# Optimization experiments

Measured on AMD Instinct MI355X. Metric: run time of the kernel, lower is better.

The kernel has to match this reference:

```python
import jax, jax.numpy as jnp
import numpy as np

B, H, W, C = 8, 256, 256, 64
M1, M2 = 16, 16
WIDTH = 64
W_SCALE = 0.02  # mimics he-normal-ish init magnitude for complex spectral weights


def setup_inputs() -> dict:
    key = jax.random.key(0)
    k1, k2, k3 = jax.random.split(key, 3)
    x = jax.random.normal(k1, (B, H, W, C), dtype=jnp.float32)
    w_real = jax.random.normal(k2, (M1, M2, C, WIDTH), dtype=jnp.float32)
    w_imag = jax.random.normal(k3, (M1, M2, C, WIDTH), dtype=jnp.float32)
    return {"x": x, "w_real": w_real, "w_imag": w_imag}


def reference(x, w_real, w_imag):
    # complex spectral weights: (M1, M2, C_in, C_out)
    weights = (w_real + 1j * w_imag) * W_SCALE
    spatial = x.shape[1:-1]  # (H, W)
    # full real FFT over spatial axes -> (B, H, W//2+1, C) complex
    x_ft = jnp.fft.rfftn(x, axes=(1, 2))
    # truncate to low-frequency modes
    x_m = x_ft[:, :M1, :M2, :]  # (B, M1, M2, C)
    # per-mode channel mixing (broadcast-ellipsis einsum in the original)
    out_m = jnp.einsum("bxyi,xyio->bxyo", x_m, weights)  # (B, M1, M2, WIDTH)
    # zero-pad back to full spectral grid
    pad = ((0, 0), (0, x_ft.shape[1] - M1), (0, x_ft.shape[2] - M2), (0, 0))
    out_ft = jnp.pad(out_m, pad, mode="constant")
    # inverse real FFT back to spatial domain
    out = jnp.fft.irfftn(out_ft, s=spatial, axes=(1, 2))  # (B, H, W, WIDTH)
    return out
```

## Files before the change

### kernel.cpp

```cpp
#include <hip/hip_runtime.h>


#define NB 8
#define NH 256
#define NW 256
#define NC 64
#define NM 16
#define NO 64

__global__ __launch_bounds__(256) void k_dft_w(const float* __restrict__ x,
                                               float* __restrict__ Gr, float* __restrict__ Gi) {
  __shared__ float2 cs[256];
  __shared__ float xs[4 * 1040];
  const int t = threadIdx.x;
  const int b = blockIdx.x >> 6;
  const int h0 = (blockIdx.x & 63) * 4;
  {
    float s, c;
    sincospif((float)t * (1.0f / 128.0f), &s, &c);
    cs[t] = make_float2(c, s);
  }
  const int i4 = t & 15;
  const int hs = (t >> 4) & 3;
  const int kyq = t >> 6;

  float4 ar[4], ai[4];
#pragma unroll
  for (int q = 0; q < 4; ++q) { ar[q] = make_float4(0, 0, 0, 0); ai[q] = make_float4(0, 0, 0, 0); }
  float stepr[4], stepi[4], twr[4], twi[4];

  const float* xb = x + (((size_t)b * NH + h0) * NW) * NC;

  for (int ch = 0; ch < 16; ++ch) {
    const int w0 = ch * 16;
    __syncthreads();
#pragma unroll
    for (int r = 0; r < 4; ++r) {
      const float4* src = (const float4*)(xb + ((size_t)r * NW + w0) * NC);
      ((float4*)xs)[r * 260 + t] = src[t];
    }
    __syncthreads();
    if (ch == 0) {
#pragma unroll
      for (int q = 0; q < 4; ++q) {
        const int ky = kyq * 4 + q;
        float2 st = cs[ky];
        stepr[q] = st.x; stepi[q] = -st.y;
      }
    }
#pragma unroll
    for (int q = 0; q < 4; ++q) {
      const int ky = kyq * 4 + q;
      float2 tv = cs[(ky * w0) & 255];
      twr[q] = tv.x; twi[q] = -tv.y;
    }
#pragma unroll 4
    for (int ww = 0; ww < 16; ++ww) {
      float4 xv = ((const float4*)xs)[hs * 260 + ww * 16 + i4];
#pragma unroll
      for (int q = 0; q < 4; ++q) {
        ar[q].x += twr[q] * xv.x; ar[q].y += twr[q] * xv.y;
        ar[q].z += twr[q] * xv.z; ar[q].w += twr[q] * xv.w;
        ai[q].x += twi[q] * xv.x; ai[q].y += twi[q] * xv.y;
        ai[q].z += twi[q] * xv.z; ai[q].w += twi[q] * xv.w;
        float nr = twr[q] * stepr[q] - twi[q] * stepi[q];
        float ni = twr[q] * stepi[q] + twi[q] * stepr[q];
        twr[q] = nr; twi[q] = ni;
      }
    }
  }
  const int h = h0 + hs;
#pragma unroll
  for (int q = 0; q < 4; ++q) {
    const int ky = kyq * 4 + q;
    const size_t o = (((size_t)(b * NM + ky)) * NH + h) * NC + i4 * 4;
    *(float4*)(Gr + o) = ar[q];
    *(float4*)(Gi + o) = ai[q];
  }
}

__global__ __launch_bounds__(256) void k_dft_h(const float* __restrict__ Gr, const float* __restrict__ Gi,
                                               float* __restrict__ Xr, float* __restrict__ Xi) {
  __shared__ float2 cs[256];
  __shared__ float gr[64 * 36];
  __shared__ float gi[64 * 36];
  const int t = threadIdx.x;
  const int b = blockIdx.x >> 5;
  const int ky = (blockIdx.x >> 1) & 15;
  const int ih = blockIdx.x & 1;
  {
    float s, c;
    sincospif((float)t * (1.0f / 128.0f), &s, &c);
    cs[t] = make_float2(c, s);
  }
  const int kx = t >> 4;
  const int i2 = (t & 15) * 2;
  float2 xr = make_float2(0, 0), xi = make_float2(0, 0);
  float str = 0.f, sti = 0.f, twr, twi;
  const float* grb = Gr + ((size_t)(b * NM + ky)) * NH * NC + ih * 32;
  const float* gib = Gi + ((size_t)(b * NM + ky)) * NH * NC + ih * 32;
  for (int ch = 0; ch < 4; ++ch) {
    const int h0 = ch * 64;
    __syncthreads();
    for (int r = 0; r < 2; ++r) {
      const int idx = r * 256 + t;
      const int hh = idx >> 3, f4 = idx & 7;
      ((float4*)&gr[hh * 36])[f4] = *(const float4*)(grb + (size_t)(h0 + hh) * NC + f4 * 4);
      ((float4*)&gi[hh * 36])[f4] = *(const float4*)(gib + (size_t)(h0 + hh) * NC + f4 * 4);
    }
    __syncthreads();
    if (ch == 0) { float2 st = cs[kx]; str = st.x; sti = -st.y; }
    float2 tv = cs[(kx * h0) & 255];
    twr = tv.x; twi = -tv.y;
#pragma unroll 8
    for (int hh = 0; hh < 64; ++hh) {
      float2 g_r = *(const float2*)&gr[hh * 36 + i2];
      float2 g_i = *(const float2*)&gi[hh * 36 + i2];
      xr.x += twr * g_r.x - twi * g_i.x;
      xr.y += twr * g_r.y - twi * g_i.y;
      xi.x += twr * g_i.x + twi * g_r.x;
      xi.y += twr * g_i.y + twi * g_r.y;
      float nr = twr * str - twi * sti;
      float ni = twr * sti + twi * str;
      twr = nr; twi = ni;
    }
  }
  const size_t o = ((size_t)((kx * NM + ky) * NB + b)) * NC + ih * 32 + i2;
  *(float2*)(Xr + o) = xr;
  *(float2*)(Xi + o) = xi;
}

__global__ __launch_bounds__(256) void k_mix(const float* __restrict__ Xr, const float* __restrict__ Xi,
                                             const float* __restrict__ w_real, const float* __restrict__ w_imag,
                                             float* __restrict__ omr, float* __restrict__ omi) {
  __shared__ float wr[64 * 64];
  __shared__ float wi[64 * 64];
  __shared__ float2 xc[8 * 64];
  const int t = threadIdx.x;
  const int kx = blockIdx.x >> 4;
  const int ky = blockIdx.x & 15;
  const size_t wbase = (size_t)(kx * NM + ky) * 4096;
  const float4* s1 = (const float4*)(w_real + wbase);
  const float4* s2 = (const float4*)(w_imag + wbase);
#pragma unroll
  for (int r = 0; r < 4; ++r) {
    ((float4*)wr)[r * 256 + t] = s1[r * 256 + t];
    ((float4*)wi)[r * 256 + t] = s2[r * 256 + t];
  }
  const size_t xbase = (size_t)(kx * NM + ky) * 512;
  for (int idx = t; idx < 512; idx += 256)
    xc[idx] = make_float2(Xr[xbase + idx], Xi[xbase + idx]);
  __syncthreads();
  const int b = t >> 5;
  const int o2 = (t & 31) * 2;
  float r0 = 0, i0 = 0, r1 = 0, i1 = 0;
#pragma unroll 8
  for (int i = 0; i < 64; ++i) {
    float2 xv = xc[b * 64 + i];
    float2 w_r = *(const float2*)&wr[i * 64 + o2];
    float2 w_i = *(const float2*)&wi[i * 64 + o2];
    r0 += xv.x * w_r.x - xv.y * w_i.x;
    i0 += xv.x * w_i.x + xv.y * w_r.x;
    r1 += xv.x * w_r.y - xv.y * w_i.y;
    i1 += xv.x * w_i.y + xv.y * w_r.y;
  }
  const float scale = (ky == 0 ? 1.0f : 2.0f) * (0.02f / 65536.0f);
  const size_t ob = (size_t)((b * NM + kx) * NM + ky) * NO + o2;
  *(float2*)(omr + ob) = make_float2(r0 * scale, r1 * scale);
  *(float2*)(omi + ob) = make_float2(i0 * scale, i1 * scale);
}

__global__ __launch_bounds__(256) void k_idft_w(const float* __restrict__ omr, const float* __restrict__ omi,
                                                float2* __restrict__ Zc) {
  __shared__ float2 cs[256];
  const int t = threadIdx.x;
  const int b = blockIdx.x >> 5;
  const int kx = (blockIdx.x >> 1) & 15;
  const int wh = blockIdx.x & 1;
  {
    float s, c;
    sincospif((float)t * (1.0f / 128.0f), &s, &c);
    cs[t] = make_float2(c, s);
  }
  __syncthreads();
  const int o = t & 63;
  const int wv = t >> 6;
  float mr[16], mi[16];
  const size_t base = (size_t)(b * NM + kx) * (NM * NO) + o;
#pragma unroll
  for (int ky = 0; ky < 16; ++ky) {
    mr[ky] = omr[base + ky * NO];
    mi[ky] = omi[base + ky * NO];
  }
  for (int j = 0; j < 32; ++j) {
    const int w = wh * 128 + wv * 32 + j;
    const float2 st = cs[w];
    float twr = 1.0f, twi = 0.0f;
    float zr = 0.0f, zi = 0.0f;
#pragma unroll
    for (int ky = 0; ky < 16; ++ky) {
      zr += twr * mr[ky] - twi * mi[ky];
      zi += twr * mi[ky] + twi * mr[ky];
      float nr = twr * st.x - twi * st.y;
      float ni = twr * st.y + twi * st.x;
      twr = nr; twi = ni;
    }
    Zc[((size_t)(b * NW + w) * NM + kx) * NO + o] = make_float2(zr, zi);
  }
}

__global__ __launch_bounds__(256) void k_idft_h(const float2* __restrict__ Zc, float* __restrict__ out) {
  __shared__ float2 cs[256];
  __shared__ float2 zc[16 * 64];
  const int t = threadIdx.x;
  const int b = blockIdx.x >> 8;
  const int w = blockIdx.x & 255;
  {
    float s, c;
    sincospif((float)t * (1.0f / 128.0f), &s, &c);
    cs[t] = make_float2(c, s);
  }
  {
    const float4* src = (const float4*)(Zc + (size_t)(b * NW + w) * (NM * NO));
    ((float4*)zc)[t] = src[t];
    ((float4*)zc)[t + 256] = src[t + 256];
  }
  __syncthreads();
  const int i4 = t & 15;
  const int h0 = (t >> 4) * 16;
  float4 acc[16];
#pragma unroll
  for (int j = 0; j < 16; ++j) acc[j] = make_float4(0, 0, 0, 0);
  for (int kx = 0; kx < 16; ++kx) {
    const float4 za = ((const float4*)zc)[kx * 32 + i4 * 2];
    const float4 zb = ((const float4*)zc)[kx * 32 + i4 * 2 + 1];
    const float2 t0 = cs[(kx * h0) & 255];
    const float2 st = cs[kx];
    float twr = t0.x, twi = t0.y;
#pragma unroll
    for (int j = 0; j < 16; ++j) {
      acc[j].x += twr * za.x - twi * za.y;
      acc[j].y += twr * za.z - twi * za.w;
      acc[j].z += twr * zb.x - twi * zb.y;
      acc[j].w += twr * zb.z - twi * zb.w;
      float nr = twr * st.x - twi * st.y;
      float ni = twr * st.y + twi * st.x;
      twr = nr; twi = ni;
    }
  }
  float* ob = out + (((size_t)b * NH + h0) * NW + w) * NO + i4 * 4;
#pragma unroll
  for (int j = 0; j < 16; ++j) {
    *(float4*)(ob + (size_t)j * (NW * NO)) = acc[j];
  }
}

extern "C" void kernel_launch(void* const* d_in, const int* in_sizes, int n_in,
                              void* d_out, int out_size, void* d_ws, size_t ws_size,
                              hipStream_t stream) {
  const float* x = (const float*)d_in[0];
  const float* w_real = (const float*)d_in[1];
  const float* w_imag = (const float*)d_in[2];
  float* out = (float*)d_out;
  char* ws = (char*)d_ws;

  float* Gr = (float*)(ws);
  float* Gi = (float*)(ws + 8388608);
  float* Xr = (float*)(ws + 16777216);
  float* Xi = (float*)(ws + 17301504);
  float* omr = (float*)(ws + 17825792);
  float* omi = (float*)(ws + 18350080);
  float2* Zc = (float2*)(ws + 18874368);

  k_dft_w<<<dim3(512), dim3(256), 0, stream>>>(x, Gr, Gi);
  k_dft_h<<<dim3(256), dim3(256), 0, stream>>>(Gr, Gi, Xr, Xi);
  k_mix<<<dim3(256), dim3(256), 0, stream>>>(Xr, Xi, w_real, w_imag, omr, omi);
  k_idft_w<<<dim3(256), dim3(256), 0, stream>>>(omr, omi, Zc);
  k_idft_h<<<dim3(2048), dim3(256), 0, stream>>>(Zc, out);
}
```

Baseline: 333.5 us.

## Raise grid parallelism across all DFT stages with split-H partial sums

Every stage is re-partitioned to launch more blocks. The W-DFT drops its LDS staging and reads x directly with fewer modes per thread. The H-DFT is split into 8 H-chunks that write partial sums, which the mix kernel reduces. The mix and inverse kernels are split in half or quarters along output channel, W and H, and complex intermediates are interleaved and reuse workspace. The aim is better occupancy on a GPU that was under-filled with 256-block launches, at the cost of extra partial-sum traffic and reduced per-thread reuse.

Result: faster. 311.5 us (-6.6%).

```diff
diff --git a/kernel.cpp b/kernel.cpp
--- a/kernel.cpp
+++ b/kernel.cpp
@@ -11,198 +11,177 @@
 __global__ __launch_bounds__(256) void k_dft_w(const float* __restrict__ x,
                                                float* __restrict__ Gr, float* __restrict__ Gi) {
   __shared__ float2 cs[256];
-  __shared__ float xs[4 * 1040];
-  const int t = threadIdx.x;
-  const int b = blockIdx.x >> 6;
-  const int h0 = (blockIdx.x & 63) * 4;
-  {
-    float s, c;
-    sincospif((float)t * (1.0f / 128.0f), &s, &c);
-    cs[t] = make_float2(c, s);
-  }
+  const int t = threadIdx.x;
+  {
+    float s, c;
+    sincospif((float)t * (1.0f / 128.0f), &s, &c);
+    cs[t] = make_float2(c, s);
+  }
+  __syncthreads();
+  const int b = blockIdx.x >> 7;
+  const int h2 = blockIdx.x & 127;
   const int i4 = t & 15;
-  const int hs = (t >> 4) & 3;
-  const int kyq = t >> 6;
-
-  float4 ar[4], ai[4];
-#pragma unroll
-  for (int q = 0; q < 4; ++q) { ar[q] = make_float4(0, 0, 0, 0); ai[q] = make_float4(0, 0, 0, 0); }
-  float stepr[4], stepi[4], twr[4], twi[4];
-
-  const float* xb = x + (((size_t)b * NH + h0) * NW) * NC;
-
-  for (int ch = 0; ch < 16; ++ch) {
-    const int w0 = ch * 16;
-    __syncthreads();
-#pragma unroll
-    for (int r = 0; r < 4; ++r) {
-      const float4* src = (const float4*)(xb + ((size_t)r * NW + w0) * NC);
-      ((float4*)xs)[r * 260 + t] = src[t];
-    }
-    __syncthreads();
-    if (ch == 0) {
-#pragma unroll
-      for (int q = 0; q < 4; ++q) {
-        const int ky = kyq * 4 + q;
-        float2 st = cs[ky];
-        stepr[q] = st.x; stepi[q] = -st.y;
-      }
-    }
-#pragma unroll
-    for (int q = 0; q < 4; ++q) {
-      const int ky = kyq * 4 + q;
-      float2 tv = cs[(ky * w0) & 255];
-      twr[q] = tv.x; twi[q] = -tv.y;
-    }
+  const int hs = (t >> 4) & 1;
+  const int kyq = t >> 5;
+  const int ky0 = kyq * 2, ky1 = ky0 + 1;
+  const int h = h2 * 2 + hs;
+  const float* xp = x + ((size_t)(b * NH + h) * NW) * NC + i4 * 4;
+
+  float4 ar0 = {0, 0, 0, 0}, ai0 = {0, 0, 0, 0}, ar1 = {0, 0, 0, 0}, ai1 = {0, 0, 0, 0};
+  const float2 s0 = cs[ky0], s1 = cs[ky1];
+  const float s0r = s0.x, s0i = -s0.y, s1r = s1.x, s1i = -s1.y;
+
+  for (int wc = 0; wc < 8; ++wc) {
+    const int w0 = wc * 32;
+    const float2 v0 = cs[(ky0 * w0) & 255], v1 = cs[(ky1 * w0) & 255];
+    float t0r = v0.x, t0i = -v0.y, t1r = v1.x, t1i = -v1.y;
+#pragma unroll 8
+    for (int w = 0; w < 32; ++w) {
+      const float4 xv = *(const float4*)(xp + (size_t)(w0 + w) * NC);
+      ar0.x += t0r * xv.x; ar0.y += t0r * xv.y; ar0.z += t0r * xv.z; ar0.w += t0r * xv.w;
+      ai0.x += t0i * xv.x; ai0.y += t0i * xv.y; ai0.z += t0i * xv.z; ai0.w += t0i * xv.w;
+      ar1.x += t1r * xv.x; ar1.y += t1r * xv.y; ar1.z += t1r * xv.z; ar1.w += t1r * xv.w;
+      ai1.x += t1i * xv.x; ai1.y += t1i * xv.y; ai1.z += t1i * xv.z; ai1.w += t1i * xv.w;
+      float n0r = t0r * s0r - t0i * s0i, n0i = t0r * s0i + t0i * s0r;
+      float n1r = t1r * s1r - t1i * s1i, n1i = t1r * s1i + t1i * s1r;
+      t0r = n0r; t0i = n0i; t1r = n1r; t1i = n1i;
+    }
+  }
+  const size_t g0 = ((size_t)(b * NM + ky0) * NH + h) * NC + i4 * 4;
+  const size_t g1 = ((size_t)(b * NM + ky1) * NH + h) * NC + i4 * 4;
+  *(float4*)(Gr + g0) = ar0; *(float4*)(Gi + g0) = ai0;
+  *(float4*)(Gr + g1) = ar1; *(float4*)(Gi + g1) = ai1;
+}
+
+__global__ __launch_bounds__(256) void k_dft_h(const float* __restrict__ Gr, const float* __restrict__ Gi,
+                                               float* __restrict__ Xpr, float* __restrict__ Xpi) {
+  __shared__ float2 cs[256];
+  __shared__ float gr[32 * 64];
+  __shared__ float gi[32 * 64];
+  const int t = threadIdx.x;
+  {
+    float s, c;
+    sincospif((float)t * (1.0f / 128.0f), &s, &c);
+    cs[t] = make_float2(c, s);
+  }
+  const int b = blockIdx.x >> 7;
+  const int ky = (blockIdx.x >> 3) & 15;
+  const int hc = blockIdx.x & 7;
+  const float* grs = Gr + ((size_t)(b * NM + ky) * NH + hc * 32) * NC;
+  const float* gis = Gi + ((size_t)(b * NM + ky) * NH + hc * 32) * NC;
+#pragma unroll
+  for (int r = 0; r < 2; ++r) {
+    ((float4*)gr)[r * 256 + t] = ((const float4*)grs)[r * 256 + t];
+    ((float4*)gi)[r * 256 + t] = ((const float4*)gis)[r * 256 + t];
+  }
+  __syncthreads();
+  const int i4 = t & 15;
+  const int kx = t >> 4;
+  float4 xr = {0, 0, 0, 0}, xi = {0, 0, 0, 0};
+  const float2 sv = cs[kx];
+  const float str = sv.x, sti = -sv.y;
+  const float2 tv = cs[(kx * hc * 32) & 255];
+  float twr = tv.x, twi = -tv.y;
 #pragma unroll 4
-    for (int ww = 0; ww < 16; ++ww) {
-      float4 xv = ((const float4*)xs)[hs * 260 + ww * 16 + i4];
-#pragma unroll
-      for (int q = 0; q < 4; ++q) {
-        ar[q].x += twr[q] * xv.x; ar[q].y += twr[q] * xv.y;
-        ar[q].z += twr[q] * xv.z; ar[q].w += twr[q] * xv.w;
-        ai[q].x += twi[q] * xv.x; ai[q].y += twi[q] * xv.y;
-        ai[q].z += twi[q] * xv.z; ai[q].w += twi[q] * xv.w;
-        float nr = twr[q] * stepr[q] - twi[q] * stepi[q];
-        float ni = twr[q] * stepi[q] + twi[q] * stepr[q];
-        twr[q] = nr; twi[q] = ni;
-      }
-    }
-  }
-  const int h = h0 + hs;
-#pragma unroll
-  for (int q = 0; q < 4; ++q) {
-    const int ky = kyq * 4 + q;
-    const size_t o = (((size_t)(b * NM + ky)) * NH + h) * NC + i4 * 4;
-    *(float4*)(Gr + o) = ar[q];
-    *(float4*)(Gi + o) = ai[q];
-  }
-}
-
-__global__ __launch_bounds__(256) void k_dft_h(const float* __restrict__ Gr, const float* __restrict__ Gi,
-                                               float* __restrict__ Xr, float* __restrict__ Xi) {
-  __shared__ float2 cs[256];
-  __shared__ float gr[64 * 36];
-  __shared__ float gi[64 * 36];
-  const int t = threadIdx.x;
-  const int b = blockIdx.x >> 5;
+  for (int hh = 0; hh < 32; ++hh) {
+    const float4 g_r = *(const float4*)&gr[hh * 64 + i4 * 4];
+    const float4 g_i = *(const float4*)&gi[hh * 64 + i4 * 4];
+    xr.x += twr * g_r.x - twi * g_i.x;
+    xr.y += twr * g_r.y - twi * g_i.y;
+    xr.z += twr * g_r.z - twi * g_i.z;
+    xr.w += twr * g_r.w - twi * g_i.w;
+    xi.x += twr * g_i.x + twi * g_r.x;
+    xi.y += twr * g_i.y + twi * g_r.y;
+    xi.z += twr * g_i.z + twi * g_r.z;
+    xi.w += twr * g_i.w + twi * g_r.w;
+    const float nr = twr * str - twi * sti;
+    const float ni = twr * sti + twi * str;
+    twr = nr; twi = ni;
+  }
+  const size_t o = ((size_t)((hc * NM + kx) * NM + ky) * NB + b) * NC + i4 * 4;
+  *(float4*)(Xpr + o) = xr;
+  *(float4*)(Xpi + o) = xi;
+}
+
+__global__ __launch_bounds__(256) void k_mix(const float* __restrict__ Xpr, const float* __restrict__ Xpi,
+                                             const float* __restrict__ w_real, const float* __restrict__ w_imag,
+                                             float2* __restrict__ om) {
+  __shared__ float wr_s[64 * 32];
+  __shared__ float wi_s[64 * 32];
+  __shared__ float2 xc[8 * 64];
+  const int t = threadIdx.x;
+  const int kx = blockIdx.x >> 5;
   const int ky = (blockIdx.x >> 1) & 15;
-  const int ih = blockIdx.x & 1;
-  {
-    float s, c;
-    sincospif((float)t * (1.0f / 128.0f), &s, &c);
-    cs[t] = make_float2(c, s);
-  }
-  const int kx = t >> 4;
-  const int i2 = (t & 15) * 2;
-  float2 xr = make_float2(0, 0), xi = make_float2(0, 0);
-  float str = 0.f, sti = 0.f, twr, twi;
-  const float* grb = Gr + ((size_t)(b * NM + ky)) * NH * NC + ih * 32;
-  const float* gib = Gi + ((size_t)(b * NM + ky)) * NH * NC + ih * 32;
-  for (int ch = 0; ch < 4; ++ch) {
-    const int h0 = ch * 64;
-    __syncthreads();
-    for (int r = 0; r < 2; ++r) {
-      const int idx = r * 256 + t;
-      const int hh = idx >> 3, f4 = idx & 7;
-      ((float4*)&gr[hh * 36])[f4] = *(const float4*)(grb + (size_t)(h0 + hh) * NC + f4 * 4);
-      ((float4*)&gi[hh * 36])[f4] = *(const float4*)(gib + (size_t)(h0 + hh) * NC + f4 * 4);
-    }
-    __syncthreads();
-    if (ch == 0) { float2 st = cs[kx]; str = st.x; sti = -st.y; }
-    float2 tv = cs[(kx * h0) & 255];
-    twr = tv.x; twi = -tv.y;
-#pragma unroll 8
-    for (int hh = 0; hh < 64; ++hh) {
-      float2 g_r = *(const float2*)&gr[hh * 36 + i2];
-      float2 g_i = *(const float2*)&gi[hh * 36 + i2];
-      xr.x += twr * g_r.x - twi * g_i.x;
-      xr.y += twr * g_r.y - twi * g_i.y;
-      xi.x += twr * g_i.x + twi * g_r.x;
-      xi.y += twr * g_i.y + twi * g_r.y;
-      float nr = twr * str - twi * sti;
-      float ni = twr * sti + twi * str;
-      twr = nr; twi = ni;
-    }
-  }
-  const size_t o = ((size_t)((kx * NM + ky) * NB + b)) * NC + ih * 32 + i2;
-  *(float2*)(Xr + o) = xr;
-  *(float2*)(Xi + o) = xi;
-}
-
-__global__ __launch_bounds__(256) void k_mix(const float* __restrict__ Xr, const float* __restrict__ Xi,
-                                             const float* __restrict__ w_real, const float* __restrict__ w_imag,
-                                             float* __restrict__ omr, float* __restrict__ omi) {
-  __shared__ float wr[64 * 64];
-  __shared__ float wi[64 * 64];
-  __shared__ float2 xc[8 * 64];
-  const int t = threadIdx.x;
-  const int kx = blockIdx.x >> 4;
-  const int ky = blockIdx.x & 15;
-  const size_t wbase = (size_t)(kx * NM + ky) * 4096;
-  const float4* s1 = (const float4*)(w_real + wbase);
-  const float4* s2 = (const float4*)(w_imag + wbase);
-#pragma unroll
-  for (int r = 0; r < 4; ++r) {
-    ((float4*)wr)[r * 256 + t] = s1[r * 256 + t];
-    ((float4*)wi)[r * 256 + t] = s2[r * 256 + t];
-  }
-  const size_t xbase = (size_t)(kx * NM + ky) * 512;
-  for (int idx = t; idx < 512; idx += 256)
-    xc[idx] = make_float2(Xr[xbase + idx], Xi[xbase + idx]);
-  __syncthreads();
+  const int oh = blockIdx.x & 1;
+  const size_t wb = (size_t)(kx * NM + ky) * 4096 + oh * 32;
+#pragma unroll
+  for (int r = 0; r < 2; ++r) {
+    const int idx = r * 256 + t;
+    const int i = idx >> 3, f = idx & 7;
+    *(float4*)&wr_s[i * 32 + f * 4] = *(const float4*)(w_real + wb + (size_t)i * 64 + f * 4);
+    *(float4*)&wi_s[i * 32 + f * 4] = *(const float4*)(w_imag + wb + (size_t)i * 64 + f * 4);
+  }
+#pragma unroll
+  for (int r = 0; r < 2; ++r) {
+    const int idx = r * 256 + t;
+    const size_t base = (size_t)(kx * NM + ky) * 512 + idx;
+    float sr = 0.f, si = 0.f;
+#pragma unroll
+    for (int hc = 0; hc < 8; ++hc) {
+      sr += Xpr[base + (size_t)hc * 131072];
+      si += Xpi[base + (size_t)hc * 131072];
+    }
+    xc[idx] = make_float2(sr, si);
+  }
+  __syncthreads();
+  const int o = t & 31;
   const int b = t >> 5;
-  const int o2 = (t & 31) * 2;
-  float r0 = 0, i0 = 0, r1 = 0, i1 = 0;
+  float r0 = 0.f, i0 = 0.f;
 #pragma unroll 8
   for (int i = 0; i < 64; ++i) {
-    float2 xv = xc[b * 64 + i];
-    float2 w_r = *(const float2*)&wr[i * 64 + o2];
-    float2 w_i = *(const float2*)&wi[i * 64 + o2];
-    r0 += xv.x * w_r.x - xv.y * w_i.x;
-    i0 += xv.x * w_i.x + xv.y * w_r.x;
-    r1 += xv.x * w_r.y - xv.y * w_i.y;
-    i1 += xv.x * w_i.y + xv.y * w_r.y;
-  }
-  const float scale = (ky == 0 ? 1.0f : 2.0f) * (0.02f / 65536.0f);
-  const size_t ob = (size_t)((b * NM + kx) * NM + ky) * NO + o2;
-  *(float2*)(omr + ob) = make_float2(r0 * scale, r1 * scale);
-  *(float2*)(omi + ob) = make_float2(i0 * scale, i1 * scale);
-}
-
-__global__ __launch_bounds__(256) void k_idft_w(const float* __restrict__ omr, const float* __restrict__ omi,
-                                                float2* __restrict__ Zc) {
-  __shared__ float2 cs[256];
-  const int t = threadIdx.x;
-  const int b = blockIdx.x >> 5;
-  const int kx = (blockIdx.x >> 1) & 15;
-  const int wh = blockIdx.x & 1;
-  {
-    float s, c;
-    sincospif((float)t * (1.0f / 128.0f), &s, &c);
-    cs[t] = make_float2(c, s);
-  }
-  __syncthreads();
+    const float2 xv = xc[b * 64 + i];
+    const float wrv = wr_s[i * 32 + o];
+    const float wiv = wi_s[i * 32 + o];
+    r0 += xv.x * wrv - xv.y * wiv;
+    i0 += xv.x * wiv + xv.y * wrv;
+  }
+  const float sc = (ky == 0 ? 1.0f : 2.0f) * (0.02f / 65536.0f);
+  om[((size_t)(b * NM + kx) * NM + ky) * NO + oh * 32 + o] = make_float2(r0 * sc, i0 * sc);
+}
+
+__global__ __launch_bounds__(256) void k_idft_w(const float2* __restrict__ om, float2* __restrict__ Zc) {
+  __shared__ float2 cs[256];
+  const int t = threadIdx.x;
+  {
+    float s, c;
+    sincospif((float)t * (1.0f / 128.0f), &s, &c);
+    cs[t] = make_float2(c, s);
+  }
+  __syncthreads();
+  const int b = blockIdx.x >> 7;
+  const int kx = (blockIdx.x >> 3) & 15;
+  const int wq = blockIdx.x & 7;
   const int o = t & 63;
-  const int wv = t >> 6;
+  const int wg = t >> 6;
   float mr[16], mi[16];
-  const size_t base = (size_t)(b * NM + kx) * (NM * NO) + o;
-#pragma unroll
-  for (int ky = 0; ky < 16; ++ky) {
-    mr[ky] = omr[base + ky * NO];
-    mi[ky] = omi[base + ky * NO];
-  }
-  for (int j = 0; j < 32; ++j) {
-    const int w = wh * 128 + wv * 32 + j;
+  const size_t base = ((size_t)(b * NM + kx) * NM) * NO + o;
+#pragma unroll
+  for (int ky = 0; ky < NM; ++ky) {
+    const float2 v = om[base + ky * NO];
+    mr[ky] = v.x; mi[ky] = v.y;
+  }
+#pragma unroll
+  for (int j = 0; j < 8; ++j) {
+    const int w = wq * 32 + wg * 8 + j;
     const float2 st = cs[w];
     float twr = 1.0f, twi = 0.0f;
     float zr = 0.0f, zi = 0.0f;
 #pragma unroll
-    for (int ky = 0; ky < 16; ++ky) {
+    for (int ky = 0; ky < NM; ++ky) {
       zr += twr * mr[ky] - twi * mi[ky];
       zi += twr * mi[ky] + twi * mr[ky];
-      float nr = twr * st.x - twi * st.y;
-      float ni = twr * st.y + twi * st.x;
+      const float nr = twr * st.x - twi * st.y;
+      const float ni = twr * st.y + twi * st.x;
       twr = nr; twi = ni;
     }
     Zc[((size_t)(b * NW + w) * NM + kx) * NO + o] = make_float2(zr, zi);
@@ -211,46 +190,53 @@
 
 __global__ __launch_bounds__(256) void k_idft_h(const float2* __restrict__ Zc, float* __restrict__ out) {
   __shared__ float2 cs[256];
-  __shared__ float2 zc[16 * 64];
-  const int t = threadIdx.x;
-  const int b = blockIdx.x >> 8;
-  const int w = blockIdx.x & 255;
-  {
-    float s, c;
-    sincospif((float)t * (1.0f / 128.0f), &s, &c);
-    cs[t] = make_float2(c, s);
-  }
-  {
-    const float4* src = (const float4*)(Zc + (size_t)(b * NW + w) * (NM * NO));
-    ((float4*)zc)[t] = src[t];
-    ((float4*)zc)[t + 256] = src[t + 256];
+  __shared__ float zre[16 * 64];
+  __shared__ float zim[16 * 64];
+  const int t = threadIdx.x;
+  {
+    float s, c;
+    sincospif((float)t * (1.0f / 128.0f), &s, &c);
+    cs[t] = make_float2(c, s);
+  }
+  const int b = blockIdx.x >> 9;
+  const int w = (blockIdx.x >> 1) & 255;
+  const int hh = blockIdx.x & 1;
+  const float4* src = (const float4*)(Zc + (size_t)(b * NW + w) * (NM * NO));
+#pragma unroll
+  for (int r = 0; r < 2; ++r) {
+    const int idx = r * 256 + t;
+    const float4 v = src[idx];
+    ((float2*)zre)[idx] = make_float2(v.x, v.z);
+    ((float2*)zim)[idx] = make_float2(v.y, v.w);
   }
   __syncthreads();
   const int i4 = t & 15;
-  const int h0 = (t >> 4) * 16;
-  float4 acc[16];
-#pragma unroll
-  for (int j = 0; j < 16; ++j) acc[j] = make_float4(0, 0, 0, 0);
+  const int hg = t >> 4;
+  const int h0 = hh * 128 + hg * 8;
+  float4 acc[8];
+#pragma unroll
+  for (int j = 0; j < 8; ++j) acc[j] = make_float4(0, 0, 0, 0);
+#pragma unroll 4
   for (int kx = 0; kx < 16; ++kx) {
-    const float4 za = ((const float4*)zc)[kx * 32 + i4 * 2];
-    const float4 zb = ((const float4*)zc)[kx * 32 + i4 * 2 + 1];
+    const float4 zr4 = ((const float4*)zre)[kx * 16 + i4];
+    const float4 zi4 = ((const float4*)zim)[kx * 16 + i4];
     const float2 t0 = cs[(kx * h0) & 255];
     const float2 st = cs[kx];
     float twr = t0.x, twi = t0.y;
 #pragma unroll
-    for (int j = 0; j < 16; ++j) {
-      acc[j].x += twr * za.x - twi * za.y;
-      acc[j].y += twr * za.z - twi * za.w;
-      acc[j].z += twr * zb.x - twi * zb.y;
-      acc[j].w += twr * zb.z - twi * zb.w;
-      float nr = twr * st.x - twi * st.y;
-      float ni = twr * st.y + twi * st.x;
+    for (int j = 0; j < 8; ++j) {
+      acc[j].x += twr * zr4.x - twi * zi4.x;
+      acc[j].y += twr * zr4.y - twi * zi4.y;
+      acc[j].z += twr * zr4.z - twi * zi4.z;
+      acc[j].w += twr * zr4.w - twi * zi4.w;
+      const float nr = twr * st.x - twi * st.y;
+      const float ni = twr * st.y + twi * st.x;
       twr = nr; twi = ni;
     }
   }
-  float* ob = out + (((size_t)b * NH + h0) * NW + w) * NO + i4 * 4;
-#pragma unroll
-  for (int j = 0; j < 16; ++j) {
+  float* ob = out + (((size_t)(b * NH) + h0) * NW + w) * NO + i4 * 4;
+#pragma unroll
+  for (int j = 0; j < 8; ++j) {
     *(float4*)(ob + (size_t)j * (NW * NO)) = acc[j];
   }
 }
@@ -266,15 +252,14 @@
 
   float* Gr = (float*)(ws);
   float* Gi = (float*)(ws + 8388608);
-  float* Xr = (float*)(ws + 16777216);
-  float* Xi = (float*)(ws + 17301504);
-  float* omr = (float*)(ws + 17825792);
-  float* omi = (float*)(ws + 18350080);
-  float2* Zc = (float2*)(ws + 18874368);
-
-  k_dft_w<<<dim3(512), dim3(256), 0, stream>>>(x, Gr, Gi);
-  k_dft_h<<<dim3(256), dim3(256), 0, stream>>>(Gr, Gi, Xr, Xi);
-  k_mix<<<dim3(256), dim3(256), 0, stream>>>(Xr, Xi, w_real, w_imag, omr, omi);
-  k_idft_w<<<dim3(256), dim3(256), 0, stream>>>(omr, omi, Zc);
-  k_idft_h<<<dim3(2048), dim3(256), 0, stream>>>(Zc, out);
-}
+  float* Xpr = (float*)(ws + 16777216);
+  float* Xpi = (float*)(ws + 20971520);
+  float2* om = (float2*)(ws + 25165824);
+  float2* Zc = (float2*)(ws);
+
+  k_dft_w<<<dim3(1024), dim3(256), 0, stream>>>(x, Gr, Gi);
+  k_dft_h<<<dim3(1024), dim3(256), 0, stream>>>(Gr, Gi, Xpr, Xpi);
+  k_mix<<<dim3(512), dim3(256), 0, stream>>>(Xpr, Xpi, w_real, w_imag, om);
+  k_idft_w<<<dim3(1024), dim3(256), 0, stream>>>(om, Zc);
+  k_idft_h<<<dim3(4096), dim3(256), 0, stream>>>(Zc, out);
+}
```
